# Performance work log

Hardware: AMD Instinct MI355X
Metric: run time of the kernel (lower is better)

The kernel has to match this reference:

```python
import jax, jax.numpy as jnp
import numpy as np
import math

B, S, D = 2, 2048, 512
H = 8
DK = D // H  # 64


def setup_inputs() -> dict:
    key = jax.random.key(0)
    ks = jax.random.split(key, 9)
    inp = {
        "query": jax.random.normal(ks[0], (B, S, D), jnp.float32),
        "key": jax.random.normal(ks[1], (B, S, D), jnp.float32),
        "value": jax.random.normal(ks[2], (B, S, D), jnp.float32),
        "attn_weight": jax.random.normal(ks[3], (B, H, S, S), jnp.float32),
        "mask": jax.random.randint(ks[4], (B, S), 0, 2).astype(bool),
        # nn.Linear(d_model, d_model, bias=False) weights, applied as x @ W.T
        "Wq": jax.random.normal(ks[5], (D, D), jnp.float32) / math.sqrt(D),
        "Wk": jax.random.normal(ks[6], (D, D), jnp.float32) / math.sqrt(D),
        "Wv": jax.random.normal(ks[7], (D, D), jnp.float32) / math.sqrt(D),
        "Wo": jax.random.normal(ks[8], (D, D), jnp.float32) / math.sqrt(D),
    }
    return inp


def reference(query, key, value, attn_weight, mask, Wq, Wk, Wv, Wo):
    b, s, d = query.shape
    # project and split heads: [b, h, s, dk]
    def split_heads(x, W):
        return (x @ W.T).reshape(b, -1, H, DK).transpose(0, 2, 1, 3)

    q = split_heads(query, Wq)
    k = split_heads(key, Wk)
    v = split_heads(value, Wv)

    scores = jnp.einsum("bhqd,bhkd->bhqk", q, k) / math.sqrt(DK)
    # mask broadcast as [b,1,1,s]: True -> -inf over keys (applied before bias subtraction,
    # matching torch order; -inf - finite stays -inf)
    scores = jnp.where(mask[:, None, None, :], -jnp.inf, scores)
    scores = scores - attn_weight
    p_attn = jax.nn.softmax(scores, axis=-1)  # dropout p=0 (eval) -> identity
    x = jnp.einsum("bhqk,bhkd->bhqd", p_attn, v)
    x = x.transpose(0, 2, 1, 3).reshape(b, -1, H * DK)
    return x @ Wo.T
```

## Files before the change

### kernel.cpp

```cpp
#include <hip/hip_runtime.h>
#include <math.h>

typedef __bf16 bf16;
typedef __bf16 bf16x8 __attribute__((ext_vector_type(8)));
typedef float f32x4 __attribute__((ext_vector_type(4)));
typedef unsigned int u32;

#define MFMA_BF16(a, b, c) __builtin_amdgcn_mfma_f32_16x16x32_bf16((a), (b), (c), 0, 0, 0)

static constexpr int kB = 2;
static constexpr int kS = 2048;
static constexpr int kD = 512;
static constexpr int kH = 8;
static constexpr int kDK = 64;
static constexpr int kTileBytes = 8192;
static constexpr int kBhBytes = 32 * kTileBytes;

__global__ void detect_mask_kernel(const unsigned char* __restrict__ m,
                                   u32* __restrict__ bm) {
  __shared__ int sh;
  const int tid = threadIdx.x;
  if (tid == 0) sh = 0;
  __syncthreads();
  int any = 0;
  for (int i = tid; i < kB * kS; i += 256)
    if ((i & 3) != 0 && m[i] != 0) any = 1;
  if (any) atomicOr(&sh, 1);
  __syncthreads();
  const bool as_bool = (sh != 0);
  for (int wi = tid; wi < kB * kS / 32; wi += 256) {
    u32 word = 0;
    const int base = wi * 32;
    for (int j = 0; j < 32; j++) {
      const bool mv = as_bool ? (m[base + j] != 0) : (((const int*)m)[base + j] != 0);
      word |= (mv ? 1u : 0u) << j;
    }
    bm[wi] = word;
  }
}

__device__ __forceinline__ void cvt16(const float* __restrict__ p, bf16x8& v0, bf16x8& v1) {
  const float4 fA = ((const float4*)p)[0];
  const float4 fB = ((const float4*)p)[1];
  const float4 fC = ((const float4*)p)[2];
  const float4 fD = ((const float4*)p)[3];
  v0[0] = (bf16)fA.x; v0[1] = (bf16)fA.y; v0[2] = (bf16)fA.z; v0[3] = (bf16)fA.w;
  v0[4] = (bf16)fB.x; v0[5] = (bf16)fB.y; v0[6] = (bf16)fB.z; v0[7] = (bf16)fB.w;
  v1[0] = (bf16)fC.x; v1[1] = (bf16)fC.y; v1[2] = (bf16)fC.z; v1[3] = (bf16)fC.w;
  v1[4] = (bf16)fD.x; v1[5] = (bf16)fD.y; v1[6] = (bf16)fD.z; v1[7] = (bf16)fD.w;
}

template <bool A_IS_F32>
__device__ __forceinline__ void gemm_body(const void* __restrict__ Aptr,
                                          const float* __restrict__ Wptr,
                                          void* __restrict__ dst, const int mode) {
  __shared__ bf16 As[128][40];
  __shared__ bf16 Bs[128][40];

  const int tid = threadIdx.x;
  const int lane = tid & 63;
  const int w = tid >> 6;
  const int wr = w >> 1, wc = w & 1;
  const int l16 = lane & 15, g = lane >> 4;

  const int m_tile = blockIdx.x * 128;
  const int n_tile = blockIdx.y * 128;

  f32x4 acc[4][4] = {};

  const int sr = tid >> 1;
  const int sc = (tid & 1) * 16;

  for (int k0 = 0; k0 < kD; k0 += 32) {
    if constexpr (A_IS_F32) {
      const float* ap = (const float*)Aptr + (size_t)(m_tile + sr) * kD + k0 + sc;
      bf16x8 v0, v1;
      cvt16(ap, v0, v1);
      *(bf16x8*)&As[sr][sc] = v0;
      *(bf16x8*)&As[sr][sc + 8] = v1;
    } else {
      const bf16* ap = (const bf16*)Aptr + (size_t)(m_tile + sr) * kD + k0 + sc;
      *(bf16x8*)&As[sr][sc] = *(const bf16x8*)ap;
      *(bf16x8*)&As[sr][sc + 8] = *(const bf16x8*)(ap + 8);
    }
    {
      const float* bp = Wptr + (size_t)(n_tile + sr) * kD + k0 + sc;
      bf16x8 v0, v1;
      cvt16(bp, v0, v1);
      *(bf16x8*)&Bs[sr][sc] = v0;
      *(bf16x8*)&Bs[sr][sc + 8] = v1;
    }
    __syncthreads();

    bf16x8 a[4], bfr[4];
    #pragma unroll
    for (int i = 0; i < 4; i++)
      a[i] = *(const bf16x8*)&As[wr * 64 + i * 16 + l16][g * 8];
    #pragma unroll
    for (int i = 0; i < 4; i++)
      bfr[i] = *(const bf16x8*)&Bs[wc * 64 + i * 16 + l16][g * 8];
    #pragma unroll
    for (int mi = 0; mi < 4; mi++)
      #pragma unroll
      for (int ni = 0; ni < 4; ni++)
        acc[mi][ni] = MFMA_BF16(a[mi], bfr[ni], acc[mi][ni]);
    __syncthreads();
  }

  #pragma unroll
  for (int mi = 0; mi < 4; mi++) {
    #pragma unroll
    for (int ni = 0; ni < 4; ni++) {
      const int gm0 = m_tile + wr * 64 + mi * 16 + g * 4;
      const int gn = n_tile + wc * 64 + ni * 16 + l16;
      #pragma unroll
      for (int q = 0; q < 4; q++) {
        const int gm = gm0 + q;
        const float v = acc[mi][ni][q];
        if (mode == 3) {
          ((float*)dst)[(size_t)gm * kD + gn] = v;
        } else {
          const int bi = gm >> 11;
          const int s = gm & (kS - 1);
          const int h = gn >> 6;
          const int dk = gn & (kDK - 1);
          if (mode == 0) {
            ((bf16*)dst)[(((size_t)bi * kH + h) * kS + s) * kDK + dk] = (bf16)v;
          } else {
            char* base = (char*)dst + (size_t)(bi * kH + h) * kBhBytes + (s >> 6) * kTileBytes;
            if (mode == 1) {
              *(bf16*)(base + (s & 63) * 128 + ((dk * 2) ^ ((s & 7) << 4))) = (bf16)v;
            } else {
              *(bf16*)(base + dk * 128 + ((((s & 63) * 2)) ^ ((dk & 7) << 4))) = (bf16)v;
            }
          }
        }
      }
    }
  }
}

__global__ __launch_bounds__(256) void proj_kernel(
    const float* __restrict__ q, const float* __restrict__ k, const float* __restrict__ v,
    const float* __restrict__ Wq, const float* __restrict__ Wk, const float* __restrict__ Wv,
    bf16* __restrict__ qw, bf16* __restrict__ kw, bf16* __restrict__ vtw) {
  const int z = blockIdx.z;
  const float* A = (z == 0) ? q : (z == 1) ? k : v;
  const float* W = (z == 0) ? Wq : (z == 1) ? Wk : Wv;
  bf16* dstp = (z == 0) ? qw : (z == 1) ? kw : vtw;
  gemm_body<true>(A, W, dstp, z);
}

__global__ __launch_bounds__(256) void out_kernel(const bf16* __restrict__ x,
                                                  const float* __restrict__ Wo,
                                                  float* __restrict__ out) {
  gemm_body<false>(x, Wo, out, 3);
}

__global__ __launch_bounds__(512, 2) void attn_kernel(
    const bf16* __restrict__ qw, const char* __restrict__ kw,
    const char* __restrict__ vt, const float* __restrict__ bias,
    const u32* __restrict__ bmask, bf16* __restrict__ xw) {
  __shared__ char KV[2][2][kTileBytes];
  __shared__ u32 Ps[8][16][36];
  __shared__ u32 mask_lds[64];

  const int tid = threadIdx.x;
  const int lane = tid & 63;
  const int w = tid >> 6;
  const int l16 = lane & 15, g = lane >> 4;

  const int bid = blockIdx.x;
  const int xcd = bid & 7;
  const int j = bid >> 3;
  const int bh = xcd * 2 + (j >> 4);
  const int qblk = j & 15;
  const int b = bh >> 3;
  const int hh = bh & 7;
  const int qr0 = qblk * 128 + w * 16;

  if (tid < 64) mask_lds[tid] = bmask[b * 64 + tid];
  __syncthreads();

  const bf16* qrow = qw + ((size_t)bh * kS + qr0 + l16) * kDK;
  const bf16x8 aq0 = *(const bf16x8*)(qrow + g * 8);
  const bf16x8 aq1 = *(const bf16x8*)(qrow + 32 + g * 8);

  const float* brow = bias + ((size_t)bh * kS + qr0 + l16) * kS;
  const char* ktile = kw + (size_t)bh * kBhBytes;
  const char* vtile = vt + (size_t)bh * kBhBytes;

  f32x4 o[4] = {};
  float m_run = -__builtin_inff();
  float l_run = 0.f;
  const int swz = (l16 & 7) << 4;

  auto dma_tile = [&](int tile, int nb) {
    const char* kg = ktile + (size_t)tile * kTileBytes + w * 1024 + lane * 16;
    __builtin_amdgcn_global_load_lds(
        (const __attribute__((address_space(1))) void*)kg,
        (__attribute__((address_space(3))) void*)&KV[nb][0][w * 1024], 16, 0, 0);
    const char* vg = vtile + (size_t)tile * kTileBytes + w * 1024 + lane * 16;
    __builtin_amdgcn_global_load_lds(
        (const __attribute__((address_space(1))) void*)vg,
        (__attribute__((address_space(3))) void*)&KV[nb][1][w * 1024], 16, 0, 0);
  };
  auto load_bias_asm = [&](f32x4 (&bv)[4], int tile) {
    const float* p0 = brow + tile * 64 + g * 4;
    asm volatile("global_load_dwordx4 %0, %1, off" : "=v"(bv[0]) : "v"(p0));
    asm volatile("global_load_dwordx4 %0, %1, off" : "=v"(bv[1]) : "v"(p0 + 16));
    asm volatile("global_load_dwordx4 %0, %1, off" : "=v"(bv[2]) : "v"(p0 + 32));
    asm volatile("global_load_dwordx4 %0, %1, off" : "=v"(bv[3]) : "v"(p0 + 48));
  };

  auto phase = [&](int t, f32x4 (&bc)[4], f32x4 (&bn)[4]) {
    const int cur = t & 1, nxt = cur ^ 1;
    const int tp = (t + 1) & 31;
    dma_tile(tp, nxt);
    load_bias_asm(bn, tp);

    const char* kb0 = &KV[cur][0][0];
    const char* vb0 = &KV[cur][1][0];
    bf16x8 kf[4][2];
    #pragma unroll
    for (int nf = 0; nf < 4; nf++) {
      const int r = nf * 16 + l16;
      #pragma unroll
      for (int h = 0; h < 2; h++)
        kf[nf][h] = *(const bf16x8*)(kb0 + r * 128 + ((g * 16 + h * 64) ^ swz));
    }
    bf16x8 vf[2][4];
    #pragma unroll
    for (int kb2 = 0; kb2 < 2; kb2++)
      #pragma unroll
      for (int ni = 0; ni < 4; ni++) {
        const int d = ni * 16 + l16;
        vf[kb2][ni] = *(const bf16x8*)(vb0 + d * 128 + ((kb2 * 64 + g * 16) ^ swz));
      }

    const u32 w0 = mask_lds[2 * t];
    const u32 w1 = mask_lds[2 * t + 1];

    f32x4 sf[4];
    __builtin_amdgcn_s_setprio(1);
    #pragma unroll
    for (int nf = 0; nf < 4; nf++) {
      f32x4 z = {};
      z = MFMA_BF16(kf[nf][0], aq0, z);
      z = MFMA_BF16(kf[nf][1], aq1, z);
      sf[nf] = z;
    }
    __builtin_amdgcn_s_setprio(0);

    asm volatile("s_waitcnt vmcnt(6)" ::: "memory");
    __builtin_amdgcn_sched_barrier(0);

    float p[4][4];
    float tmax = -__builtin_inff();
    #pragma unroll
    for (int nf = 0; nf < 4; nf++) {
      const u32 wsel = (nf < 2) ? w0 : w1;
      #pragma unroll
      for (int r = 0; r < 4; r++) {
        float sv = sf[nf][r] * 0.125f - bc[nf][r];
        const int bp = (nf & 1) * 16 + g * 4 + r;
        if ((wsel >> bp) & 1) sv = -__builtin_inff();
        p[nf][r] = sv;
        tmax = fmaxf(tmax, sv);
      }
    }
    tmax = fmaxf(tmax, __shfl_xor(tmax, 16, 64));
    tmax = fmaxf(tmax, __shfl_xor(tmax, 32, 64));

    const float mnew = fmaxf(m_run, tmax);
    const float scale = (m_run == -__builtin_inff()) ? 0.f : __expf(m_run - mnew);
    const float mexp = (mnew == -__builtin_inff()) ? 0.f : mnew;
    float psum = 0.f;
    #pragma unroll
    for (int nf = 0; nf < 4; nf++)
      #pragma unroll
      for (int r = 0; r < 4; r++) {
        const float pv = __expf(p[nf][r] - mexp);
        p[nf][r] = pv;
        psum += pv;
      }
    psum += __shfl_xor(psum, 16, 64);
    psum += __shfl_xor(psum, 32, 64);
    m_run = mnew;
    l_run = l_run * scale + psum;
    #pragma unroll
    for (int ni = 0; ni < 4; ni++) o[ni] *= scale;

    #pragma unroll
    for (int nf = 0; nf < 4; nf++) {
      union { bf16 h[2]; u32 u; } c0, c1;
      c0.h[0] = (bf16)p[nf][0]; c0.h[1] = (bf16)p[nf][1];
      c1.h[0] = (bf16)p[nf][2]; c1.h[1] = (bf16)p[nf][3];
      Ps[w][l16][nf * 8 + g * 2] = c0.u;
      Ps[w][l16][nf * 8 + g * 2 + 1] = c1.u;
    }
    asm volatile("s_waitcnt lgkmcnt(0)" ::: "memory");

    __builtin_amdgcn_s_setprio(1);
    #pragma unroll
    for (int kb2 = 0; kb2 < 2; kb2++) {
      const bf16x8 pb = *(const bf16x8*)&Ps[w][l16][kb2 * 16 + g * 4];
      #pragma unroll
      for (int ni = 0; ni < 4; ni++)
        o[ni] = MFMA_BF16(vf[kb2][ni], pb, o[ni]);
    }
    __builtin_amdgcn_s_setprio(0);

    asm volatile("s_waitcnt vmcnt(4)" ::: "memory");
    __builtin_amdgcn_s_barrier();
    __builtin_amdgcn_sched_barrier(0);
  };

  f32x4 bc[4], bn[4];
  dma_tile(0, 0);
  load_bias_asm(bc, 0);
  asm volatile("s_waitcnt vmcnt(4)" ::: "memory");
  __builtin_amdgcn_s_barrier();
  __builtin_amdgcn_sched_barrier(0);

  for (int t = 0; t < 32; t += 2) {
    phase(t, bc, bn);
    phase(t + 1, bn, bc);
  }

  const float inv = (l_run > 0.f) ? 1.f / l_run : 0.f;
  bf16* dstp = xw + ((size_t)b * kS + qr0 + l16) * kD + hh * kDK;
  #pragma unroll
  for (int ni = 0; ni < 4; ni++) {
    union { bf16 h[2]; u32 u; } c0, c1;
    c0.h[0] = (bf16)(o[ni][0] * inv); c0.h[1] = (bf16)(o[ni][1] * inv);
    c1.h[0] = (bf16)(o[ni][2] * inv); c1.h[1] = (bf16)(o[ni][3] * inv);
    *(u32*)&dstp[ni * 16 + g * 4] = c0.u;
    *(u32*)&dstp[ni * 16 + g * 4 + 2] = c1.u;
  }
}

extern "C" void kernel_launch(void* const* d_in, const int* in_sizes, int n_in,
                              void* d_out, int out_size, void* d_ws, size_t ws_size,
                              hipStream_t stream) {
  (void)in_sizes; (void)n_in; (void)out_size; (void)ws_size;
  const float* query = (const float*)d_in[0];
  const float* key_in = (const float*)d_in[1];
  const float* value = (const float*)d_in[2];
  const float* attnw = (const float*)d_in[3];
  const unsigned char* mask = (const unsigned char*)d_in[4];
  const float* Wq = (const float*)d_in[5];
  const float* Wk = (const float*)d_in[6];
  const float* Wv = (const float*)d_in[7];
  const float* Wo = (const float*)d_in[8];

  const size_t nqkv = (size_t)kB * kH * kS * kDK;
  size_t off = 0;
  auto alloc = [&](size_t bytes) {
    void* p = (char*)d_ws + off;
    off = (off + bytes + 255) & ~(size_t)255;
    return p;
  };
  u32* bm = (u32*)alloc(kB * kS / 32 * 4);
  bf16* q_ws = (bf16*)alloc(nqkv * 2);
  char* k_ws = (char*)alloc(nqkv * 2);
  char* vt_ws = (char*)alloc(nqkv * 2);
  bf16* x_ws = (bf16*)alloc((size_t)kB * kS * kD * 2);

  detect_mask_kernel<<<1, 256, 0, stream>>>(mask, bm);

  proj_kernel<<<dim3(32, 4, 3), dim3(256), 0, stream>>>(query, key_in, value, Wq, Wk, Wv,
                                                        q_ws, (bf16*)k_ws, (bf16*)vt_ws);
  attn_kernel<<<dim3(256), dim3(512), 0, stream>>>(q_ws, k_ws, vt_ws, attnw, bm, x_ws);
  out_kernel<<<dim3(32, 4), dim3(256), 0, stream>>>(x_ws, Wo, (float*)d_out);
}
```

Baseline: 151.0 us.

## Vectorize projection epilogue stores and halve attention block size

```diff
diff --git a/kernel.cpp b/kernel.cpp
--- a/kernel.cpp
+++ b/kernel.cpp
@@ -5,6 +5,7 @@
 typedef __bf16 bf16x8 __attribute__((ext_vector_type(8)));
 typedef float f32x4 __attribute__((ext_vector_type(4)));
 typedef unsigned int u32;
+typedef unsigned long long u64;
 
 #define MFMA_BF16(a, b, c) __builtin_amdgcn_mfma_f32_16x16x32_bf16((a), (b), (c), 0, 0, 0)
 
@@ -50,10 +51,11 @@
   v1[4] = (bf16)fD.x; v1[5] = (bf16)fD.y; v1[6] = (bf16)fD.z; v1[7] = (bf16)fD.w;
 }
 
-template <bool A_IS_F32>
+template <bool A_IS_F32, int MODE>
 __device__ __forceinline__ void gemm_body(const void* __restrict__ Aptr,
                                           const float* __restrict__ Wptr,
-                                          void* __restrict__ dst, const int mode) {
+                                          void* __restrict__ dst) {
+  constexpr bool TRANS = (MODE != 2);
   __shared__ bf16 As[128][40];
   __shared__ bf16 Bs[128][40];
 
@@ -102,8 +104,12 @@
     #pragma unroll
     for (int mi = 0; mi < 4; mi++)
       #pragma unroll
-      for (int ni = 0; ni < 4; ni++)
-        acc[mi][ni] = MFMA_BF16(a[mi], bfr[ni], acc[mi][ni]);
+      for (int ni = 0; ni < 4; ni++) {
+        if constexpr (TRANS)
+          acc[mi][ni] = MFMA_BF16(bfr[ni], a[mi], acc[mi][ni]);
+        else
+          acc[mi][ni] = MFMA_BF16(a[mi], bfr[ni], acc[mi][ni]);
+      }
     __syncthreads();
   }
 
@@ -111,30 +117,40 @@
   for (int mi = 0; mi < 4; mi++) {
     #pragma unroll
     for (int ni = 0; ni < 4; ni++) {
-      const int gm0 = m_tile + wr * 64 + mi * 16 + g * 4;
-      const int gn = n_tile + wc * 64 + ni * 16 + l16;
-      #pragma unroll
-      for (int q = 0; q < 4; q++) {
-        const int gm = gm0 + q;
-        const float v = acc[mi][ni][q];
-        if (mode == 3) {
-          ((float*)dst)[(size_t)gm * kD + gn] = v;
+      const f32x4 v = acc[mi][ni];
+      if constexpr (TRANS) {
+        const int gm = m_tile + wr * 64 + mi * 16 + l16;
+        const int gn0 = n_tile + wc * 64 + ni * 16 + g * 4;
+        if constexpr (MODE == 3) {
+          *(float4*)&((float*)dst)[(size_t)gm * kD + gn0] =
+              (float4){v[0], v[1], v[2], v[3]};
         } else {
           const int bi = gm >> 11;
           const int s = gm & (kS - 1);
-          const int h = gn >> 6;
-          const int dk = gn & (kDK - 1);
-          if (mode == 0) {
-            ((bf16*)dst)[(((size_t)bi * kH + h) * kS + s) * kDK + dk] = (bf16)v;
+          const int h = gn0 >> 6;
+          const int dk0 = gn0 & (kDK - 1);
+          union { bf16 hh[4]; u64 u; } pk;
+          pk.hh[0] = (bf16)v[0]; pk.hh[1] = (bf16)v[1];
+          pk.hh[2] = (bf16)v[2]; pk.hh[3] = (bf16)v[3];
+          if constexpr (MODE == 0) {
+            *(u64*)&((bf16*)dst)[(((size_t)bi * kH + h) * kS + s) * kDK + dk0] = pk.u;
           } else {
             char* base = (char*)dst + (size_t)(bi * kH + h) * kBhBytes + (s >> 6) * kTileBytes;
-            if (mode == 1) {
-              *(bf16*)(base + (s & 63) * 128 + ((dk * 2) ^ ((s & 7) << 4))) = (bf16)v;
-            } else {
-              *(bf16*)(base + dk * 128 + ((((s & 63) * 2)) ^ ((dk & 7) << 4))) = (bf16)v;
-            }
+            *(u64*)(base + (s & 63) * 128 + ((dk0 * 2) ^ ((s & 7) << 4))) = pk.u;
           }
         }
+      } else {
+        const int gm0 = m_tile + wr * 64 + mi * 16 + g * 4;
+        const int gn = n_tile + wc * 64 + ni * 16 + l16;
+        const int bi = gm0 >> 11;
+        const int s0 = gm0 & (kS - 1);
+        const int h = gn >> 6;
+        const int dk = gn & (kDK - 1);
+        union { bf16 hh[4]; u64 u; } pk;
+        pk.hh[0] = (bf16)v[0]; pk.hh[1] = (bf16)v[1];
+        pk.hh[2] = (bf16)v[2]; pk.hh[3] = (bf16)v[3];
+        char* base = (char*)dst + (size_t)(bi * kH + h) * kBhBytes + (s0 >> 6) * kTileBytes;
+        *(u64*)(base + dk * 128 + (((s0 & 63) * 2) ^ ((dk & 7) << 4))) = pk.u;
       }
     }
   }
@@ -145,24 +161,23 @@
     const float* __restrict__ Wq, const float* __restrict__ Wk, const float* __restrict__ Wv,
     bf16* __restrict__ qw, bf16* __restrict__ kw, bf16* __restrict__ vtw) {
   const int z = blockIdx.z;
-  const float* A = (z == 0) ? q : (z == 1) ? k : v;
-  const float* W = (z == 0) ? Wq : (z == 1) ? Wk : Wv;
-  bf16* dstp = (z == 0) ? qw : (z == 1) ? kw : vtw;
-  gemm_body<true>(A, W, dstp, z);
+  if (z == 0) gemm_body<true, 0>(q, Wq, qw);
+  else if (z == 1) gemm_body<true, 1>(k, Wk, kw);
+  else gemm_body<true, 2>(v, Wv, vtw);
 }
 
 __global__ __launch_bounds__(256) void out_kernel(const bf16* __restrict__ x,
                                                   const float* __restrict__ Wo,
                                                   float* __restrict__ out) {
-  gemm_body<false>(x, Wo, out, 3);
-}
-
-__global__ __launch_bounds__(512, 2) void attn_kernel(
+  gemm_body<false, 3>(x, Wo, out);
+}
+
+__global__ __launch_bounds__(256, 2) void attn_kernel(
     const bf16* __restrict__ qw, const char* __restrict__ kw,
     const char* __restrict__ vt, const float* __restrict__ bias,
     const u32* __restrict__ bmask, bf16* __restrict__ xw) {
   __shared__ char KV[2][2][kTileBytes];
-  __shared__ u32 Ps[8][16][36];
+  __shared__ u32 Ps[4][16][36];
   __shared__ u32 mask_lds[64];
 
   const int tid = threadIdx.x;
@@ -173,11 +188,11 @@
   const int bid = blockIdx.x;
   const int xcd = bid & 7;
   const int j = bid >> 3;
-  const int bh = xcd * 2 + (j >> 4);
-  const int qblk = j & 15;
+  const int bh = xcd * 2 + (j >> 5);
+  const int qb = j & 31;
   const int b = bh >> 3;
   const int hh = bh & 7;
-  const int qr0 = qblk * 128 + w * 16;
+  const int qr0 = qb * 64 + w * 16;
 
   if (tid < 64) mask_lds[tid] = bmask[b * 64 + tid];
   __syncthreads();
@@ -196,14 +211,20 @@
   const int swz = (l16 & 7) << 4;
 
   auto dma_tile = [&](int tile, int nb) {
-    const char* kg = ktile + (size_t)tile * kTileBytes + w * 1024 + lane * 16;
+    const char* kg = ktile + (size_t)tile * kTileBytes + w * 2048 + lane * 16;
     __builtin_amdgcn_global_load_lds(
         (const __attribute__((address_space(1))) void*)kg,
-        (__attribute__((address_space(3))) void*)&KV[nb][0][w * 1024], 16, 0, 0);
-    const char* vg = vtile + (size_t)tile * kTileBytes + w * 1024 + lane * 16;
+        (__attribute__((address_space(3))) void*)&KV[nb][0][w * 2048], 16, 0, 0);
+    __builtin_amdgcn_global_load_lds(
+        (const __attribute__((address_space(1))) void*)(kg + 1024),
+        (__attribute__((address_space(3))) void*)&KV[nb][0][w * 2048 + 1024], 16, 0, 0);
+    const char* vg = vtile + (size_t)tile * kTileBytes + w * 2048 + lane * 16;
     __builtin_amdgcn_global_load_lds(
         (const __attribute__((address_space(1))) void*)vg,
-        (__attribute__((address_space(3))) void*)&KV[nb][1][w * 1024], 16, 0, 0);
+        (__attribute__((address_space(3))) void*)&KV[nb][1][w * 2048], 16, 0, 0);
+    __builtin_amdgcn_global_load_lds(
+        (const __attribute__((address_space(1))) void*)(vg + 1024),
+        (__attribute__((address_space(3))) void*)&KV[nb][1][w * 2048 + 1024], 16, 0, 0);
   };
   auto load_bias_asm = [&](f32x4 (&bv)[4], int tile) {
     const float* p0 = brow + tile * 64 + g * 4;
@@ -252,7 +273,7 @@
     }
     __builtin_amdgcn_s_setprio(0);
 
-    asm volatile("s_waitcnt vmcnt(6)" ::: "memory");
+    asm volatile("s_waitcnt vmcnt(8)" ::: "memory");
     __builtin_amdgcn_sched_barrier(0);
 
     float p[4][4];
@@ -371,6 +392,6 @@
 
   proj_kernel<<<dim3(32, 4, 3), dim3(256), 0, stream>>>(query, key_in, value, Wq, Wk, Wv,
                                                         q_ws, (bf16*)k_ws, (bf16*)vt_ws);
-  attn_kernel<<<dim3(256), dim3(512), 0, stream>>>(q_ws, k_ws, vt_ws, attnw, bm, x_ws);
+  attn_kernel<<<dim3(512), dim3(256), 0, stream>>>(q_ws, k_ws, vt_ws, attnw, bm, x_ws);
   out_kernel<<<dim3(32, 4), dim3(256), 0, stream>>>(x_ws, Wo, (float*)d_out);
 }
```

After: 141.7 us. 1.07x faster.
